# Kernel tuning notes

Measured on AMD Instinct MI355X. Metric: run time of the kernel, lower is better.

## Reference

```python
import jax, jax.numpy as jnp
import numpy as np

SHAPE = (4096, 4096)
TAU = 1.0
EPS = 1e-8


def setup_inputs() -> dict:
    key = jax.random.key(0)
    k1, k2, k3 = jax.random.split(key, 3)
    mask_logits = 0.1 * jax.random.normal(k1, SHAPE, dtype=jnp.float32)
    u1 = jax.random.uniform(k2, SHAPE, dtype=jnp.float32)
    u2 = jax.random.uniform(k3, SHAPE + (2,), dtype=jnp.float32)
    return {"mask_logits": mask_logits, "u1": u1, "u2": u2,
            "k": 1677721, "training": 1}


def _gumbel(u):
    # -log(-log(U + eps) + eps), matching the torch code's noise
    return -jnp.log(-jnp.log(u + EPS) + EPS)


def reference(mask_logits, u1, u2, k, training):
    shape = mask_logits.shape
    if training:
        # gumbel-perturbed logits
        logits_with_noise = (mask_logits + _gumbel(u1)) / TAU
        flat = logits_with_noise.reshape(-1)                 # [N]
        _, top_idx = jax.lax.top_k(flat, k)                  # [k]
        # scatter: binary candidate mask (constant values -> non-diff, as in torch)
        mask = jnp.zeros_like(flat).at[top_idx].set(1.0)     # [N]
        # F.gumbel_softmax(stack([0, mask], -1), tau, hard=True)[..., 1]
        logits2 = jnp.stack([jnp.zeros_like(mask), mask], axis=-1)   # [N, 2]
        g2 = _gumbel(u2.reshape(-1, 2))                      # [N, 2]
        y = jax.nn.softmax((logits2 + g2) / TAU, axis=-1)    # soft sample
        hard = jax.nn.one_hot(jnp.argmax(y, axis=-1), 2, dtype=y.dtype)
        out = (hard + y - jax.lax.stop_gradient(y))[..., 1]  # straight-through
        return out.reshape(shape)
    else:
        flat = mask_logits.reshape(-1)
        _, top_idx = jax.lax.top_k(flat, k)
        mask = jnp.zeros_like(flat).at[top_idx].set(1.0)
        return mask.reshape(shape)
```

## Files before the change

kernel.cpp:

```cpp
#include <hip/hip_runtime.h>
#include <hip/hip_bf16.h>
#include <math.h>
#include <cstdint>

#define FEPS 1e-8f
#define NTHR 256
#define CAND_CAP 4096
#define NREP 32

#define GRID_KEYS 2048
#define GRID_H2   2048
#define GRID_FIN  2048
#define GRID_PART 1024

#define ZMIN 8.0f
#define ZSCALE 128.0f
#define ZBINW 0.0078125f


__device__ __forceinline__ uint32_t f2k(float f) {
    uint32_t b = __float_as_uint(f);
    return (b & 0x80000000u) ? ~b : (b | 0x80000000u);
}

__device__ __forceinline__ float gum_fast(float u) {
    float t = u + FEPS;
    float a = logf(t);
    float w = -a + FEPS;
    float d = logf(w);
    return -d;
}

__device__ __forceinline__ float logCR(float x) {
    return (float)log((double)x);
}
__device__ __forceinline__ float gum_cr(float u) {
    float t = u + FEPS;
    float a = logCR(t);
    float w = -a + FEPS;
    float d = logCR(w);
    return -d;
}

__device__ __forceinline__ float decide_cr(float maskv, float ua, float ub) {
    float G0 = gum_cr(ua);
    float G1 = gum_cr(ub);
    float V1 = maskv + G1;
    float diff = V1 - G0;
    return (diff > 0x1p-25f) ? 1.0f : 0.0f;
}

__device__ __forceinline__ float decide_fast(float mv, float ua, float ub) {
    float w0 = -logf(ua + FEPS) + FEPS;
    float w1 = -logf(ub + FEPS) + FEPS;
    float T = (mv != 0.0f) ? 0.36787944f : 1.0f;
    float rhs = T * w1;
    float q = w0 - rhs;
    if (fabsf(q) > 1e-4f * rhs) return (q > 0.0f) ? 1.0f : 0.0f;
    return decide_cr(mv, ua, ub);
}

__device__ __forceinline__ int zbin(float z) {
    float t = (z + ZMIN) * ZSCALE;
    int b = (int)t;
    if (b < 0) b = 0;
    if (b > 4095) b = 4095;
    return b;
}

__global__ void k_zero(uint32_t* __restrict__ hist1r, uint32_t* __restrict__ hist2,
                       uint32_t* __restrict__ scal, uint32_t* __restrict__ candCount) {
    int i = blockIdx.x * blockDim.x + threadIdx.x;
    int stride = gridDim.x * blockDim.x;
    for (int b = i; b < NREP * 4096; b += stride) hist1r[b] = 0u;
    for (int b = i; b < (1 << 20); b += stride) hist2[b] = 0u;
    if (i < 16) scal[i] = 0u;
    if (i == 0) *candCount = 0u;
}

__global__ void __launch_bounds__(NTHR) k_keys(
        const float* __restrict__ lg, const float* __restrict__ u1,
        const int* __restrict__ trainp, uint32_t* __restrict__ keys,
        uint32_t* __restrict__ hist1r, int N) {
    __shared__ uint32_t h[4096];
    for (int b = threadIdx.x; b < 4096; b += NTHR) h[b] = 0u;
    __syncthreads();
    const int tr = *trainp;
    const int n4 = N >> 2;
    const int nth = gridDim.x * NTHR;
    const float4* lg4 = (const float4*)lg;
    const float4* u14 = (const float4*)u1;
    uint4* k4 = (uint4*)keys;

    int p0 = blockIdx.x * NTHR + threadIdx.x;
    while (p0 + nth < n4) {
        const int p1 = p0 + nth;
        float4 m0 = lg4[p0];
        float4 m1 = lg4[p1];
        float4 a0 = u14[p0];
        float4 a1 = u14[p1];
        float z0, z1, z2, z3, z4, z5, z6, z7;
        if (tr) {
            z0 = m0.x + gum_fast(a0.x); z1 = m0.y + gum_fast(a0.y);
            z2 = m0.z + gum_fast(a0.z); z3 = m0.w + gum_fast(a0.w);
            z4 = m1.x + gum_fast(a1.x); z5 = m1.y + gum_fast(a1.y);
            z6 = m1.z + gum_fast(a1.z); z7 = m1.w + gum_fast(a1.w);
        } else {
            z0 = m0.x; z1 = m0.y; z2 = m0.z; z3 = m0.w;
            z4 = m1.x; z5 = m1.y; z6 = m1.z; z7 = m1.w;
        }
        k4[p0] = make_uint4(f2k(z0), f2k(z1), f2k(z2), f2k(z3));
        k4[p1] = make_uint4(f2k(z4), f2k(z5), f2k(z6), f2k(z7));
        atomicAdd(&h[zbin(z0)], 1u); atomicAdd(&h[zbin(z1)], 1u);
        atomicAdd(&h[zbin(z2)], 1u); atomicAdd(&h[zbin(z3)], 1u);
        atomicAdd(&h[zbin(z4)], 1u); atomicAdd(&h[zbin(z5)], 1u);
        atomicAdd(&h[zbin(z6)], 1u); atomicAdd(&h[zbin(z7)], 1u);
        p0 += 2 * nth;
    }
    if (p0 < n4) {
        float4 m0 = lg4[p0];
        float4 a0 = u14[p0];
        float z0, z1, z2, z3;
        if (tr) {
            z0 = m0.x + gum_fast(a0.x); z1 = m0.y + gum_fast(a0.y);
            z2 = m0.z + gum_fast(a0.z); z3 = m0.w + gum_fast(a0.w);
        } else { z0 = m0.x; z1 = m0.y; z2 = m0.z; z3 = m0.w; }
        k4[p0] = make_uint4(f2k(z0), f2k(z1), f2k(z2), f2k(z3));
        atomicAdd(&h[zbin(z0)], 1u); atomicAdd(&h[zbin(z1)], 1u);
        atomicAdd(&h[zbin(z2)], 1u); atomicAdd(&h[zbin(z3)], 1u);
    }
    for (int i = (n4 << 2) + blockIdx.x * NTHR + threadIdx.x; i < N; i += nth) {
        float m = lg[i], u = u1[i];
        float z = tr ? (m + gum_fast(u)) : m;
        keys[i] = f2k(z);
        atomicAdd(&h[zbin(z)], 1u);
    }
    __syncthreads();
    uint32_t* rep = hist1r + (uint32_t)(blockIdx.x & (NREP - 1)) * 4096u;
    for (int b = threadIdx.x; b < 4096; b += NTHR) {
        uint32_t v = h[b];
        if (v) atomicAdd(&rep[b], v);
    }
}

__global__ void __launch_bounds__(1024) k_scan1(
        const uint32_t* __restrict__ hist1r, const int* __restrict__ kptr,
        uint32_t* __restrict__ scal) {
    __shared__ uint32_t vals[4096];
    __shared__ uint32_t cnt[1024];
    const int t = threadIdx.x;
    uint32_t loc = 0;
    for (int j = 0; j < 4; j++) {
        const int bin = 4095 - (t * 4 + j);
        uint32_t v = 0;
        #pragma unroll
        for (int r = 0; r < NREP; r++) v += hist1r[r * 4096 + bin];
        vals[t * 4 + j] = v;
        loc += v;
    }
    cnt[t] = loc;
    __syncthreads();
    for (int off = 1; off < 1024; off <<= 1) {
        uint32_t add = (t >= off) ? cnt[t - off] : 0u;
        __syncthreads();
        cnt[t] += add;
        __syncthreads();
    }
    const uint32_t K = (uint32_t)(*kptr);
    uint32_t excl = (t > 0) ? cnt[t - 1] : 0u;
    uint32_t incl = cnt[t];
    if (excl < K && K <= incl) {
        uint32_t c = excl;
        for (int j = 0; j < 4; j++) {
            uint32_t v = vals[t * 4 + j];
            if (K <= c + v) {
                int b1 = 4095 - (t * 4 + j);
                float edge = (float)b1 * ZBINW - ZMIN;
                uint32_t kb = f2k(edge) - 2048u;
                scal[0] = kb;
                break;
            }
            c += v;
        }
    }
}

__global__ void __launch_bounds__(NTHR) k_hist2(
        const uint32_t* __restrict__ keys, const uint32_t* __restrict__ scal,
        uint32_t* __restrict__ hist2, uint32_t* __restrict__ gtOut, int N) {
    __shared__ uint32_t red[NTHR];
    const uint32_t kb = scal[0];
    const uint32_t hiB = kb + (1u << 20);
    const int n4 = N >> 2;
    const int tid = blockIdx.x * NTHR + threadIdx.x;
    const int stride = gridDim.x * NTHR;
    const uint4* k4 = (const uint4*)keys;
    uint32_t gt = 0;
    for (int i = tid; i < n4; i += stride) {
        uint4 kk = k4[i];
        uint32_t ks[4] = {kk.x, kk.y, kk.z, kk.w};
        #pragma unroll
        for (int j = 0; j < 4; j++) {
            uint32_t kx = ks[j];
            if (kx >= hiB) gt++;
            else if (kx >= kb) atomicAdd(&hist2[kx - kb], 1u);
        }
    }
    for (int i = (n4 << 2) + tid; i < N; i += stride) {
        uint32_t kx = keys[i];
        if (kx >= hiB) gt++;
        else if (kx >= kb) atomicAdd(&hist2[kx - kb], 1u);
    }
    red[threadIdx.x] = gt;
    __syncthreads();
    for (int off = NTHR / 2; off; off >>= 1) {
        if (threadIdx.x < off) red[threadIdx.x] += red[threadIdx.x + off];
        __syncthreads();
    }
    if (threadIdx.x == 0 && red[0]) atomicAdd(gtOut, red[0]);
}

__global__ void __launch_bounds__(NTHR) k_part(
        const uint32_t* __restrict__ hist2, uint32_t* __restrict__ part) {
    __shared__ uint32_t red[NTHR];
    uint32_t sum = 0;
    const int base = blockIdx.x << 10;
    for (int j = threadIdx.x; j < 1024; j += NTHR) sum += hist2[base + j];
    red[threadIdx.x] = sum;
    __syncthreads();
    for (int off = NTHR / 2; off; off >>= 1) {
        if (threadIdx.x < off) red[threadIdx.x] += red[threadIdx.x + off];
        __syncthreads();
    }
    if (threadIdx.x == 0) part[blockIdx.x] = red[0];
}

__global__ void __launch_bounds__(1024) k_scan2(
        const uint32_t* __restrict__ hist2, const uint32_t* __restrict__ part,
        const int* __restrict__ kptr, uint32_t* __restrict__ scal) {
    __shared__ uint32_t cs[1024];
    __shared__ uint32_t bs[1024];
    __shared__ uint32_t red[1024];
    __shared__ int shI[4];
    const int t = threadIdx.x;
    const uint32_t kb = scal[0];
    const uint32_t GT = scal[1];
    const uint32_t kk1 = (uint32_t)(*kptr) - GT;

    cs[t] = part[1023 - t];
    __syncthreads();
    for (int off = 1; off < 1024; off <<= 1) {
        uint32_t add = (t >= off) ? cs[t - off] : 0u;
        __syncthreads();
        cs[t] += add;
        __syncthreads();
    }
    {
        uint32_t excl = t ? cs[t - 1] : 0u;
        if (excl < kk1 && kk1 <= cs[t]) shI[0] = t;
    }
    __syncthreads();
    const int rp = shI[0];
    const int jc = 1023 - rp;
    const uint32_t gt_chunks = rp ? cs[rp - 1] : 0u;
    const uint32_t kk_in = kk1 - gt_chunks;

    bs[t] = hist2[(jc << 10) + (1023 - t)];
    __syncthreads();
    for (int off = 1; off < 1024; off <<= 1) {
        uint32_t add = (t >= off) ? bs[t - off] : 0u;
        __syncthreads();
        bs[t] += add;
        __syncthreads();
    }
    {
        uint32_t excl = t ? bs[t - 1] : 0u;
        if (excl < kk_in && kk_in <= bs[t]) shI[1] = t;
    }
    __syncthreads();
    const int rq = shI[1];
    const int b2 = (jc << 10) + (1023 - rq);

    int W = 64;
    int lo = 0, hi = 0;
    uint32_t caw = 0;
    while (true) {
        lo = b2 - W; if (lo < 0) lo = 0;
        hi = b2 + W; if (hi > 0xFFFFF) hi = 0xFFFFF;
        uint32_t v = 0;
        for (int b = lo + t; b <= hi; b += 1024) v += hist2[b];
        red[t] = v;
        __syncthreads();
        for (int off = 512; off; off >>= 1) {
            if (t < off) red[t] += red[t + off];
            __syncthreads();
        }
        uint32_t nW = red[0];
        __syncthreads();
        if (nW <= 3500u || W == 0) {
            const int ch = hi >> 10;
            const int chend = (ch << 10) + 1023;
            uint32_t v2 = 0;
            for (int b = hi + 1 + t; b <= chend; b += 1024) v2 += hist2[b];
            red[t] = v2;
            __syncthreads();
            for (int off = 512; off; off >>= 1) {
                if (t < off) red[t] += red[t + off];
                __syncthreads();
            }
            uint32_t inpart = red[0];
            __syncthreads();
            const int rpch = 1023 - ch;
            const uint32_t sufExcl = rpch ? cs[rpch - 1] : 0u;
            caw = GT + sufExcl + inpart;
            break;
        }
        W >>= 1;
    }
    if (t == 0) {
        scal[3] = kb + (uint32_t)lo;
        scal[4] = kb + (uint32_t)hi;
        scal[5] = caw;
    }
}

__global__ void __launch_bounds__(NTHR) k_final(
        uint32_t* __restrict__ keys ,
        const float* __restrict__ u2, const int* __restrict__ trainp,
        const uint32_t* __restrict__ scal,
        uint32_t* __restrict__ candIdx, uint32_t* __restrict__ candCount, int N) {
    const uint32_t klo = scal[3], khi = scal[4];
    const int tr = *trainp;
    const int n4 = N >> 2;
    const int tid = blockIdx.x * NTHR + threadIdx.x;
    const int stride = gridDim.x * NTHR;
    const uint4* kr4 = (const uint4*)keys;
    const float4* u24 = (const float4*)u2;
    float* outf = (float*)keys;

    for (int i = tid; i < n4; i += stride) {
        uint4 kk = kr4[i];
        uint32_t ks[4] = {kk.x, kk.y, kk.z, kk.w};
        float uu[8];
        if (tr) {
            float4 ua = u24[2 * i];
            float4 ub = u24[2 * i + 1];
            uu[0] = ua.x; uu[1] = ua.y; uu[2] = ua.z; uu[3] = ua.w;
            uu[4] = ub.x; uu[5] = ub.y; uu[6] = ub.z; uu[7] = ub.w;
        }
        float res[4];
        bool inw[4];
        bool anyw = false;
        #pragma unroll
        for (int j = 0; j < 4; j++) {
            inw[j] = (ks[j] >= klo) && (ks[j] <= khi);
            anyw |= inw[j];
        }
        #pragma unroll
        for (int j = 0; j < 4; j++) {
            float mv = (ks[j] > khi) ? 1.0f : 0.0f;
            res[j] = (tr && !inw[j]) ? decide_fast(mv, uu[2 * j], uu[2 * j + 1]) : mv;
        }
        if (!anyw) {
            ((float4*)outf)[i] = make_float4(res[0], res[1], res[2], res[3]);
        } else {
            #pragma unroll
            for (int j = 0; j < 4; j++) {
                if (inw[j]) {
                    uint32_t p = atomicAdd(candCount, 1u);
                    if (p < CAND_CAP) candIdx[p] = (uint32_t)(4 * i + j);
                } else {
                    outf[4 * i + j] = res[j];
                }
            }
        }
    }
    for (int i = (n4 << 2) + tid; i < N; i += stride) {
        uint32_t kx = keys[i];
        if (kx >= klo && kx <= khi) {
            uint32_t p = atomicAdd(candCount, 1u);
            if (p < CAND_CAP) candIdx[p] = (uint32_t)i;
            continue;
        }
        float mv = (kx > khi) ? 1.0f : 0.0f;
        outf[i] = tr ? decide_fast(mv, u2[2 * i], u2[2 * i + 1]) : mv;
    }
}

__global__ void __launch_bounds__(NTHR) k_refine(
        const float* __restrict__ lg, const float* __restrict__ u1,
        const float* __restrict__ u2, const int* __restrict__ kptr,
        const int* __restrict__ trainp, const uint32_t* __restrict__ scal,
        const uint32_t* __restrict__ candIdx, const uint32_t* __restrict__ candCount,
        float* __restrict__ out) {
    __shared__ float zs[CAND_CAP];
    __shared__ int is[CAND_CAP];
    const int tr = *trainp;
    int n = (int)(*candCount);
    if (n > CAND_CAP) n = CAND_CAP;
    int npow2 = 64;
    while (npow2 < n) npow2 <<= 1;

    for (int e = threadIdx.x; e < npow2; e += NTHR) {
        if (e < n) {
            int i = (int)candIdx[e];
            float m = lg[i];
            zs[e] = tr ? (m + gum_cr(u1[i])) : m;
            is[e] = i;
        } else {
            zs[e] = -INFINITY;
            is[e] = 0x40000000 + e;
        }
    }
    __syncthreads();

    for (int size = 2; size <= npow2; size <<= 1) {
        for (int str = size >> 1; str > 0; str >>= 1) {
            for (int e = threadIdx.x; e < npow2; e += NTHR) {
                int p = e ^ str;
                if (p > e) {
                    float za = zs[e], zb = zs[p];
                    int ia = is[e], ib = is[p];
                    bool aBefore = (za > zb) || (za == zb && ia < ib);
                    bool descBlock = ((e & size) == 0);
                    if (descBlock ? !aBefore : aBefore) {
                        zs[e] = zb; zs[p] = za;
                        is[e] = ib; is[p] = ia;
                    }
                }
            }
            __syncthreads();
        }
    }

    const int K = *kptr;
    const int caw = (int)scal[5];
    const int R = K - caw;
    for (int e = threadIdx.x; e < n; e += NTHR) {
        int i = is[e];
        float mv = (e < R) ? 1.0f : 0.0f;
        out[i] = tr ? decide_cr(mv, u2[2 * i], u2[2 * i + 1]) : mv;
    }
}

extern "C" void kernel_launch(void* const* d_in, const int* in_sizes, int n_in,
                              void* d_out, int out_size, void* d_ws, size_t ws_size,
                              hipStream_t stream) {
    const float* lg = (const float*)d_in[0];
    const float* u1 = (const float*)d_in[1];
    const float* u2 = (const float*)d_in[2];
    const int* kptr = (const int*)d_in[3];
    const int* trainp = (const int*)d_in[4];
    float* out = (float*)d_out;
    const int N = in_sizes[0];

    uint32_t* keys = (uint32_t*)d_out;

    uint32_t* hist1r = (uint32_t*)d_ws;
    uint32_t* hist2 = hist1r + NREP * 4096;
    uint32_t* part = hist2 + (1u << 20);
    uint32_t* scal = part + 1024;
    uint32_t* candCount = scal + 16;
    uint32_t* candIdx = candCount + 1;

    k_zero<<<dim3(1024), dim3(NTHR), 0, stream>>>(hist1r, hist2, scal, candCount);
    k_keys<<<dim3(GRID_KEYS), dim3(NTHR), 0, stream>>>(lg, u1, trainp, keys, hist1r, N);
    k_scan1<<<dim3(1), dim3(1024), 0, stream>>>(hist1r, kptr, scal);
    k_hist2<<<dim3(GRID_H2), dim3(NTHR), 0, stream>>>(keys, scal, hist2, &scal[1], N);
    k_part<<<dim3(GRID_PART), dim3(NTHR), 0, stream>>>(hist2, part);
    k_scan2<<<dim3(1), dim3(1024), 0, stream>>>(hist2, part, kptr, scal);
    k_final<<<dim3(GRID_FIN), dim3(NTHR), 0, stream>>>(keys, u2, trainp, scal,
                                                       candIdx, candCount, N);
    k_refine<<<dim3(1), dim3(NTHR), 0, stream>>>(lg, u1, u2, kptr, trainp, scal,
                                                 candIdx, candCount, out);
}
```

Before: 164.6 us.

## Replace full key pass with sampled histogram, 2-bit class map, and recompute

The first histogram pass now samples 1/16 of the elements to estimate the threshold bin, scaled by K/16. It no longer writes full 32-bit keys. A second pass recomputes the Gumbel values with a fast approximate log and classifies each element as above, below, or near the threshold, storing a 2-bit class map. It refines exactly only inside a band, and the smaller 2^17 histogram drops the partial-sum kernel. The final pass decides clear cases from raw uniform comparisons and recomputes keys only for near-threshold elements, trading memory traffic for recomputation. The risk is sampling error: if the true threshold falls outside the chosen 2^17-key window, the result is wrong.

```diff
diff --git a/kernel.cpp b/kernel.cpp
--- a/kernel.cpp
+++ b/kernel.cpp
@@ -7,11 +7,13 @@
 #define NTHR 256
 #define CAND_CAP 4096
 #define NREP 32
-
-#define GRID_KEYS 2048
-#define GRID_H2   2048
-#define GRID_FIN  2048
-#define GRID_PART 1024
+#define H2BITS 17
+#define H2SIZE (1u << H2BITS)
+#define BAND 3e-3f
+#define UCMP 1e-3f
+
+#define GRID_MAP 2048
+#define GRID_FIN 2048
 
 #define ZMIN 8.0f
 #define ZSCALE 128.0f
@@ -21,43 +23,54 @@
 __device__ __forceinline__ uint32_t f2k(float f) {
     uint32_t b = __float_as_uint(f);
     return (b & 0x80000000u) ? ~b : (b | 0x80000000u);
+}
+__device__ __forceinline__ float k2f(uint32_t k) {
+    uint32_t b = (k & 0x80000000u) ? (k & 0x7FFFFFFFu) : ~k;
+    return __uint_as_float(b);
 }
 
 __device__ __forceinline__ float gum_fast(float u) {
     float t = u + FEPS;
     float a = logf(t);
     float w = -a + FEPS;
-    float d = logf(w);
-    return -d;
-}
-
-__device__ __forceinline__ float logCR(float x) {
-    return (float)log((double)x);
-}
+    return -logf(w);
+}
+__device__ __forceinline__ float gum_scr(float u) {
+    float t = u + FEPS;
+    float a = __logf(t);
+    float w = -a + FEPS;
+    return -__logf(w);
+}
+
+__device__ __forceinline__ float logCR(float x) { return (float)log((double)x); }
 __device__ __forceinline__ float gum_cr(float u) {
     float t = u + FEPS;
     float a = logCR(t);
     float w = -a + FEPS;
-    float d = logCR(w);
-    return -d;
+    return -logCR(w);
 }
 
 __device__ __forceinline__ float decide_cr(float maskv, float ua, float ub) {
     float G0 = gum_cr(ua);
     float G1 = gum_cr(ub);
-    float V1 = maskv + G1;
-    float diff = V1 - G0;
+    float diff = (maskv + G1) - G0;
     return (diff > 0x1p-25f) ? 1.0f : 0.0f;
 }
 
 __device__ __forceinline__ float decide_fast(float mv, float ua, float ub) {
-    float w0 = -logf(ua + FEPS) + FEPS;
-    float w1 = -logf(ub + FEPS) + FEPS;
+    float w0 = -__logf(ua + FEPS) + FEPS;
+    float w1 = -__logf(ub + FEPS) + FEPS;
     float T = (mv != 0.0f) ? 0.36787944f : 1.0f;
     float rhs = T * w1;
     float q = w0 - rhs;
     if (fabsf(q) > 1e-4f * rhs) return (q > 0.0f) ? 1.0f : 0.0f;
     return decide_cr(mv, ua, ub);
+}
+
+__device__ __forceinline__ float decide0(float ua, float ub) {
+    float d = ub - ua;
+    if (fabsf(d) > UCMP) return (d > 0.0f) ? 1.0f : 0.0f;
+    return decide_fast(0.0f, ua, ub);
 }
 
 __device__ __forceinline__ int zbin(float z) {
@@ -73,67 +86,35 @@
     int i = blockIdx.x * blockDim.x + threadIdx.x;
     int stride = gridDim.x * blockDim.x;
     for (int b = i; b < NREP * 4096; b += stride) hist1r[b] = 0u;
-    for (int b = i; b < (1 << 20); b += stride) hist2[b] = 0u;
+    for (uint32_t b = i; b < H2SIZE; b += stride) hist2[b] = 0u;
     if (i < 16) scal[i] = 0u;
     if (i == 0) *candCount = 0u;
 }
 
-__global__ void __launch_bounds__(NTHR) k_keys(
+__global__ void __launch_bounds__(NTHR) k_samp(
         const float* __restrict__ lg, const float* __restrict__ u1,
-        const int* __restrict__ trainp, uint32_t* __restrict__ keys,
-        uint32_t* __restrict__ hist1r, int N) {
+        const int* __restrict__ trainp, uint32_t* __restrict__ hist1r, int N) {
     __shared__ uint32_t h[4096];
     for (int b = threadIdx.x; b < 4096; b += NTHR) h[b] = 0u;
     __syncthreads();
     const int tr = *trainp;
     const int n4 = N >> 2;
-    const int nth = gridDim.x * NTHR;
+    const int gtid = blockIdx.x * NTHR + threadIdx.x;
     const float4* lg4 = (const float4*)lg;
     const float4* u14 = (const float4*)u1;
-    uint4* k4 = (uint4*)keys;
-
-    int p0 = blockIdx.x * NTHR + threadIdx.x;
-    while (p0 + nth < n4) {
-        const int p1 = p0 + nth;
-        float4 m0 = lg4[p0];
-        float4 m1 = lg4[p1];
-        float4 a0 = u14[p0];
-        float4 a1 = u14[p1];
-        float z0, z1, z2, z3, z4, z5, z6, z7;
-        if (tr) {
-            z0 = m0.x + gum_fast(a0.x); z1 = m0.y + gum_fast(a0.y);
-            z2 = m0.z + gum_fast(a0.z); z3 = m0.w + gum_fast(a0.w);
-            z4 = m1.x + gum_fast(a1.x); z5 = m1.y + gum_fast(a1.y);
-            z6 = m1.z + gum_fast(a1.z); z7 = m1.w + gum_fast(a1.w);
-        } else {
-            z0 = m0.x; z1 = m0.y; z2 = m0.z; z3 = m0.w;
-            z4 = m1.x; z5 = m1.y; z6 = m1.z; z7 = m1.w;
-        }
-        k4[p0] = make_uint4(f2k(z0), f2k(z1), f2k(z2), f2k(z3));
-        k4[p1] = make_uint4(f2k(z4), f2k(z5), f2k(z6), f2k(z7));
-        atomicAdd(&h[zbin(z0)], 1u); atomicAdd(&h[zbin(z1)], 1u);
-        atomicAdd(&h[zbin(z2)], 1u); atomicAdd(&h[zbin(z3)], 1u);
-        atomicAdd(&h[zbin(z4)], 1u); atomicAdd(&h[zbin(z5)], 1u);
-        atomicAdd(&h[zbin(z6)], 1u); atomicAdd(&h[zbin(z7)], 1u);
-        p0 += 2 * nth;
-    }
-    if (p0 < n4) {
-        float4 m0 = lg4[p0];
-        float4 a0 = u14[p0];
-        float z0, z1, z2, z3;
-        if (tr) {
-            z0 = m0.x + gum_fast(a0.x); z1 = m0.y + gum_fast(a0.y);
-            z2 = m0.z + gum_fast(a0.z); z3 = m0.w + gum_fast(a0.w);
-        } else { z0 = m0.x; z1 = m0.y; z2 = m0.z; z3 = m0.w; }
-        k4[p0] = make_uint4(f2k(z0), f2k(z1), f2k(z2), f2k(z3));
-        atomicAdd(&h[zbin(z0)], 1u); atomicAdd(&h[zbin(z1)], 1u);
-        atomicAdd(&h[zbin(z2)], 1u); atomicAdd(&h[zbin(z3)], 1u);
-    }
-    for (int i = (n4 << 2) + blockIdx.x * NTHR + threadIdx.x; i < N; i += nth) {
-        float m = lg[i], u = u1[i];
-        float z = tr ? (m + gum_fast(u)) : m;
-        keys[i] = f2k(z);
-        atomicAdd(&h[zbin(z)], 1u);
+    #pragma unroll
+    for (int q = 0; q < 4; q++) {
+        int pos = (gtid + q * 65536) << 4;
+        if (pos < n4) {
+            float4 m = lg4[pos];
+            float4 u = u14[pos];
+            float z0 = tr ? m.x + gum_scr(u.x) : m.x;
+            float z1 = tr ? m.y + gum_scr(u.y) : m.y;
+            float z2 = tr ? m.z + gum_scr(u.z) : m.z;
+            float z3 = tr ? m.w + gum_scr(u.w) : m.w;
+            atomicAdd(&h[zbin(z0)], 1u); atomicAdd(&h[zbin(z1)], 1u);
+            atomicAdd(&h[zbin(z2)], 1u); atomicAdd(&h[zbin(z3)], 1u);
+        }
     }
     __syncthreads();
     uint32_t* rep = hist1r + (uint32_t)(blockIdx.x & (NREP - 1)) * 4096u;
@@ -166,18 +147,24 @@
         cnt[t] += add;
         __syncthreads();
     }
-    const uint32_t K = (uint32_t)(*kptr);
-    uint32_t excl = (t > 0) ? cnt[t - 1] : 0u;
-    uint32_t incl = cnt[t];
-    if (excl < K && K <= incl) {
-        uint32_t c = excl;
+    const float Kf = (float)(*kptr) * 0.0625f;
+    float excl = (t > 0) ? (float)cnt[t - 1] : 0.0f;
+    float incl = (float)cnt[t];
+    if (excl < Kf && Kf <= incl) {
+        float c = excl;
         for (int j = 0; j < 4; j++) {
-            uint32_t v = vals[t * 4 + j];
-            if (K <= c + v) {
+            float v = (float)vals[t * 4 + j];
+            if (Kf <= c + v) {
                 int b1 = 4095 - (t * 4 + j);
-                float edge = (float)b1 * ZBINW - ZMIN;
-                uint32_t kb = f2k(edge) - 2048u;
+                int bmar = b1 - 2;
+                if (bmar < 0) bmar = 0;
+                float elo = (float)bmar * ZBINW - ZMIN;
+                uint32_t kb = f2k(elo);
                 scal[0] = kb;
+                float zlo = k2f(kb) - BAND;
+                float zhi = k2f(kb + H2SIZE) + BAND;
+                scal[6] = __float_as_uint(zlo);
+                scal[7] = __float_as_uint(zhi);
                 break;
             }
             c += v;
@@ -185,31 +172,75 @@
     }
 }
 
-__global__ void __launch_bounds__(NTHR) k_hist2(
-        const uint32_t* __restrict__ keys, const uint32_t* __restrict__ scal,
-        uint32_t* __restrict__ hist2, uint32_t* __restrict__ gtOut, int N) {
+__global__ void __launch_bounds__(NTHR) k_map(
+        const float* __restrict__ lg, const float* __restrict__ u1,
+        const int* __restrict__ trainp, const uint32_t* __restrict__ scal_ro,
+        uint32_t* __restrict__ hist2, uint32_t* __restrict__ scal,
+        unsigned char* __restrict__ map, int N) {
     __shared__ uint32_t red[NTHR];
-    const uint32_t kb = scal[0];
-    const uint32_t hiB = kb + (1u << 20);
+    const int tr = *trainp;
+    const uint32_t kb = scal_ro[0];
+    const uint32_t hiB = kb + H2SIZE;
+    const float zlo_scr = __uint_as_float(scal_ro[6]);
+    const float zhi_scr = __uint_as_float(scal_ro[7]);
     const int n4 = N >> 2;
-    const int tid = blockIdx.x * NTHR + threadIdx.x;
-    const int stride = gridDim.x * NTHR;
-    const uint4* k4 = (const uint4*)keys;
+    const int nth = gridDim.x * NTHR;
+    const float4* lg4 = (const float4*)lg;
+    const float4* u14 = (const float4*)u1;
     uint32_t gt = 0;
-    for (int i = tid; i < n4; i += stride) {
-        uint4 kk = k4[i];
-        uint32_t ks[4] = {kk.x, kk.y, kk.z, kk.w};
+
+    int p0 = blockIdx.x * NTHR + threadIdx.x;
+    while (p0 + nth < n4) {
+        const int p1 = p0 + nth;
+        float4 m0 = lg4[p0];
+        float4 m1 = lg4[p1];
+        float4 a0 = u14[p0];
+        float4 a1 = u14[p1];
+        float ms[8] = {m0.x, m0.y, m0.z, m0.w, m1.x, m1.y, m1.z, m1.w};
+        float us[8] = {a0.x, a0.y, a0.z, a0.w, a1.x, a1.y, a1.z, a1.w};
+        unsigned int bc0 = 0, bc1 = 0;
+        #pragma unroll
+        for (int j = 0; j < 8; j++) {
+            float zh = tr ? ms[j] + gum_scr(us[j]) : ms[j];
+            uint32_t cls;
+            if (zh > zhi_scr) { cls = 1u; gt++; }
+            else if (zh < zlo_scr) cls = 0u;
+            else {
+                float ze = tr ? ms[j] + gum_fast(us[j]) : ms[j];
+                uint32_t key = f2k(ze);
+                if (key >= hiB) { cls = 1u; gt++; }
+                else if (key >= kb) { atomicAdd(&hist2[key - kb], 1u); cls = 2u; }
+                else cls = 0u;
+            }
+            if (j < 4) bc0 |= cls << (2 * j);
+            else bc1 |= cls << (2 * (j - 4));
+        }
+        map[p0] = (unsigned char)bc0;
+        map[p1] = (unsigned char)bc1;
+        p0 += 2 * nth;
+    }
+    if (p0 < n4) {
+        float4 m0 = lg4[p0];
+        float4 a0 = u14[p0];
+        float ms[4] = {m0.x, m0.y, m0.z, m0.w};
+        float us[4] = {a0.x, a0.y, a0.z, a0.w};
+        unsigned int bc0 = 0;
         #pragma unroll
         for (int j = 0; j < 4; j++) {
-            uint32_t kx = ks[j];
-            if (kx >= hiB) gt++;
-            else if (kx >= kb) atomicAdd(&hist2[kx - kb], 1u);
-        }
-    }
-    for (int i = (n4 << 2) + tid; i < N; i += stride) {
-        uint32_t kx = keys[i];
-        if (kx >= hiB) gt++;
-        else if (kx >= kb) atomicAdd(&hist2[kx - kb], 1u);
+            float zh = tr ? ms[j] + gum_scr(us[j]) : ms[j];
+            uint32_t cls;
+            if (zh > zhi_scr) { cls = 1u; gt++; }
+            else if (zh < zlo_scr) cls = 0u;
+            else {
+                float ze = tr ? ms[j] + gum_fast(us[j]) : ms[j];
+                uint32_t key = f2k(ze);
+                if (key >= hiB) { cls = 1u; gt++; }
+                else if (key >= kb) { atomicAdd(&hist2[key - kb], 1u); cls = 2u; }
+                else cls = 0u;
+            }
+            bc0 |= cls << (2 * j);
+        }
+        map[p0] = (unsigned char)bc0;
     }
     red[threadIdx.x] = gt;
     __syncthreads();
@@ -217,55 +248,44 @@
         if (threadIdx.x < off) red[threadIdx.x] += red[threadIdx.x + off];
         __syncthreads();
     }
-    if (threadIdx.x == 0 && red[0]) atomicAdd(gtOut, red[0]);
-}
-
-__global__ void __launch_bounds__(NTHR) k_part(
-        const uint32_t* __restrict__ hist2, uint32_t* __restrict__ part) {
-    __shared__ uint32_t red[NTHR];
-    uint32_t sum = 0;
-    const int base = blockIdx.x << 10;
-    for (int j = threadIdx.x; j < 1024; j += NTHR) sum += hist2[base + j];
-    red[threadIdx.x] = sum;
-    __syncthreads();
-    for (int off = NTHR / 2; off; off >>= 1) {
-        if (threadIdx.x < off) red[threadIdx.x] += red[threadIdx.x + off];
-        __syncthreads();
-    }
-    if (threadIdx.x == 0) part[blockIdx.x] = red[0];
+    if (threadIdx.x == 0 && red[0]) atomicAdd(&scal[1], red[0]);
 }
 
 __global__ void __launch_bounds__(1024) k_scan2(
-        const uint32_t* __restrict__ hist2, const uint32_t* __restrict__ part,
-        const int* __restrict__ kptr, uint32_t* __restrict__ scal) {
-    __shared__ uint32_t cs[1024];
+        const uint32_t* __restrict__ hist2, const int* __restrict__ kptr,
+        uint32_t* __restrict__ scal) {
+    __shared__ uint32_t ss[1024];
     __shared__ uint32_t bs[1024];
     __shared__ uint32_t red[1024];
-    __shared__ int shI[4];
+    __shared__ int shI[2];
     const int t = threadIdx.x;
     const uint32_t kb = scal[0];
+    if (t < 2) shI[t] = 0;
+
+    const int s = 1023 - t;
+    uint32_t sum = 0;
+    for (int j = 0; j < 128; j++) sum += hist2[(s << 7) + j];
+    ss[t] = sum;
+    __syncthreads();
+    for (int off = 1; off < 1024; off <<= 1) {
+        uint32_t add = (t >= off) ? ss[t - off] : 0u;
+        __syncthreads();
+        ss[t] += add;
+        __syncthreads();
+    }
     const uint32_t GT = scal[1];
     const uint32_t kk1 = (uint32_t)(*kptr) - GT;
-
-    cs[t] = part[1023 - t];
-    __syncthreads();
-    for (int off = 1; off < 1024; off <<= 1) {
-        uint32_t add = (t >= off) ? cs[t - off] : 0u;
-        __syncthreads();
-        cs[t] += add;
-        __syncthreads();
-    }
     {
-        uint32_t excl = t ? cs[t - 1] : 0u;
-        if (excl < kk1 && kk1 <= cs[t]) shI[0] = t;
+        uint32_t excl = t ? ss[t - 1] : 0u;
+        if (excl < kk1 && kk1 <= ss[t]) shI[0] = t;
     }
     __syncthreads();
     const int rp = shI[0];
-    const int jc = 1023 - rp;
-    const uint32_t gt_chunks = rp ? cs[rp - 1] : 0u;
-    const uint32_t kk_in = kk1 - gt_chunks;
-
-    bs[t] = hist2[(jc << 10) + (1023 - t)];
+    const int sstrip = 1023 - rp;
+    const uint32_t gt_strips = rp ? ss[rp - 1] : 0u;
+    const uint32_t kk_in = kk1 - gt_strips;
+
+    bs[t] = (t < 128) ? hist2[(sstrip << 7) + (127 - t)] : 0u;
     __syncthreads();
     for (int off = 1; off < 1024; off <<= 1) {
         uint32_t add = (t >= off) ? bs[t - off] : 0u;
@@ -275,18 +295,18 @@
     }
     {
         uint32_t excl = t ? bs[t - 1] : 0u;
-        if (excl < kk_in && kk_in <= bs[t]) shI[1] = t;
+        if (t < 128 && excl < kk_in && kk_in <= bs[t]) shI[1] = t;
     }
     __syncthreads();
     const int rq = shI[1];
-    const int b2 = (jc << 10) + (1023 - rq);
+    const int b2 = (sstrip << 7) + (127 - rq);
 
     int W = 64;
     int lo = 0, hi = 0;
     uint32_t caw = 0;
     while (true) {
         lo = b2 - W; if (lo < 0) lo = 0;
-        hi = b2 + W; if (hi > 0xFFFFF) hi = 0xFFFFF;
+        hi = b2 + W; if (hi > (int)H2SIZE - 1) hi = (int)H2SIZE - 1;
         uint32_t v = 0;
         for (int b = lo + t; b <= hi; b += 1024) v += hist2[b];
         red[t] = v;
@@ -298,10 +318,10 @@
         uint32_t nW = red[0];
         __syncthreads();
         if (nW <= 3500u || W == 0) {
-            const int ch = hi >> 10;
-            const int chend = (ch << 10) + 1023;
+            const int hs = hi >> 7;
+            const int hend = ((hs + 1) << 7) - 1;
             uint32_t v2 = 0;
-            for (int b = hi + 1 + t; b <= chend; b += 1024) v2 += hist2[b];
+            for (int b = hi + 1 + t; b <= hend; b += 1024) v2 += hist2[b];
             red[t] = v2;
             __syncthreads();
             for (int off = 512; off; off >>= 1) {
@@ -310,9 +330,9 @@
             }
             uint32_t inpart = red[0];
             __syncthreads();
-            const int rpch = 1023 - ch;
-            const uint32_t sufExcl = rpch ? cs[rpch - 1] : 0u;
-            caw = GT + sufExcl + inpart;
+            const int rp_hs = 1023 - hs;
+            const uint32_t strips_above = rp_hs ? ss[rp_hs - 1] : 0u;
+            caw = GT + strips_above + inpart;
             break;
         }
         W >>= 1;
@@ -325,65 +345,68 @@
 }
 
 __global__ void __launch_bounds__(NTHR) k_final(
-        uint32_t* __restrict__ keys ,
+        const unsigned char* __restrict__ map,
+        const float* __restrict__ lg, const float* __restrict__ u1,
         const float* __restrict__ u2, const int* __restrict__ trainp,
         const uint32_t* __restrict__ scal,
-        uint32_t* __restrict__ candIdx, uint32_t* __restrict__ candCount, int N) {
+        uint32_t* __restrict__ candIdx, uint32_t* __restrict__ candCount,
+        float* __restrict__ out, int N) {
     const uint32_t klo = scal[3], khi = scal[4];
     const int tr = *trainp;
     const int n4 = N >> 2;
     const int tid = blockIdx.x * NTHR + threadIdx.x;
     const int stride = gridDim.x * NTHR;
-    const uint4* kr4 = (const uint4*)keys;
     const float4* u24 = (const float4*)u2;
-    float* outf = (float*)keys;
+    const float4* lg4 = (const float4*)lg;
+    const float4* u14 = (const float4*)u1;
 
     for (int i = tid; i < n4; i += stride) {
-        uint4 kk = kr4[i];
-        uint32_t ks[4] = {kk.x, kk.y, kk.z, kk.w};
-        float uu[8];
-        if (tr) {
-            float4 ua = u24[2 * i];
-            float4 ub = u24[2 * i + 1];
-            uu[0] = ua.x; uu[1] = ua.y; uu[2] = ua.z; uu[3] = ua.w;
-            uu[4] = ub.x; uu[5] = ub.y; uu[6] = ub.z; uu[7] = ub.w;
+        const unsigned int b = map[i];
+        float4 ua4, ub4;
+        if (tr) { ua4 = u24[2 * i]; ub4 = u24[2 * i + 1]; }
+        float pa[4] = {ua4.x, ua4.z, ub4.x, ub4.z};
+        float pb[4] = {ua4.y, ua4.w, ub4.y, ub4.w};
+        const bool has2 = ((b & 3u) == 2u) | (((b >> 2) & 3u) == 2u) |
+                          (((b >> 4) & 3u) == 2u) | (((b >> 6) & 3u) == 2u);
+        float me[4], ue[4];
+        if (has2) {
+            float4 mm = lg4[i];
+            float4 uu = u14[i];
+            me[0] = mm.x; me[1] = mm.y; me[2] = mm.z; me[3] = mm.w;
+            ue[0] = uu.x; ue[1] = uu.y; ue[2] = uu.z; ue[3] = uu.w;
         }
         float res[4];
-        bool inw[4];
-        bool anyw = false;
+        bool cand[4];
+        bool anyc = false;
         #pragma unroll
         for (int j = 0; j < 4; j++) {
-            inw[j] = (ks[j] >= klo) && (ks[j] <= khi);
-            anyw |= inw[j];
-        }
-        #pragma unroll
-        for (int j = 0; j < 4; j++) {
-            float mv = (ks[j] > khi) ? 1.0f : 0.0f;
-            res[j] = (tr && !inw[j]) ? decide_fast(mv, uu[2 * j], uu[2 * j + 1]) : mv;
-        }
-        if (!anyw) {
-            ((float4*)outf)[i] = make_float4(res[0], res[1], res[2], res[3]);
+            const unsigned int cls = (b >> (2 * j)) & 3u;
+            cand[j] = false;
+            if (cls == 0u) {
+                res[j] = tr ? decide0(pa[j], pb[j]) : 0.0f;
+            } else if (cls == 1u) {
+                res[j] = tr ? decide_fast(1.0f, pa[j], pb[j]) : 1.0f;
+            } else {
+                float ze = tr ? me[j] + gum_fast(ue[j]) : me[j];
+                uint32_t key = f2k(ze);
+                if (key > khi) res[j] = tr ? decide_fast(1.0f, pa[j], pb[j]) : 1.0f;
+                else if (key < klo) res[j] = tr ? decide0(pa[j], pb[j]) : 0.0f;
+                else { cand[j] = true; anyc = true; res[j] = 0.0f; }
+            }
+        }
+        if (!anyc) {
+            ((float4*)out)[i] = make_float4(res[0], res[1], res[2], res[3]);
         } else {
             #pragma unroll
             for (int j = 0; j < 4; j++) {
-                if (inw[j]) {
+                if (cand[j]) {
                     uint32_t p = atomicAdd(candCount, 1u);
                     if (p < CAND_CAP) candIdx[p] = (uint32_t)(4 * i + j);
                 } else {
-                    outf[4 * i + j] = res[j];
+                    out[4 * i + j] = res[j];
                 }
             }
         }
-    }
-    for (int i = (n4 << 2) + tid; i < N; i += stride) {
-        uint32_t kx = keys[i];
-        if (kx >= klo && kx <= khi) {
-            uint32_t p = atomicAdd(candCount, 1u);
-            if (p < CAND_CAP) candIdx[p] = (uint32_t)i;
-            continue;
-        }
-        float mv = (kx > khi) ? 1.0f : 0.0f;
-        outf[i] = tr ? decide_fast(mv, u2[2 * i], u2[2 * i + 1]) : mv;
     }
 }
 
@@ -454,23 +477,21 @@
     float* out = (float*)d_out;
     const int N = in_sizes[0];
 
-    uint32_t* keys = (uint32_t*)d_out;
-
     uint32_t* hist1r = (uint32_t*)d_ws;
     uint32_t* hist2 = hist1r + NREP * 4096;
-    uint32_t* part = hist2 + (1u << 20);
-    uint32_t* scal = part + 1024;
+    uint32_t* scal = hist2 + H2SIZE;
     uint32_t* candCount = scal + 16;
     uint32_t* candIdx = candCount + 1;
-
-    k_zero<<<dim3(1024), dim3(NTHR), 0, stream>>>(hist1r, hist2, scal, candCount);
-    k_keys<<<dim3(GRID_KEYS), dim3(NTHR), 0, stream>>>(lg, u1, trainp, keys, hist1r, N);
+    unsigned char* map = (unsigned char*)(candIdx + CAND_CAP);
+
+    k_zero<<<dim3(256), dim3(NTHR), 0, stream>>>(hist1r, hist2, scal, candCount);
+    k_samp<<<dim3(256), dim3(NTHR), 0, stream>>>(lg, u1, trainp, hist1r, N);
     k_scan1<<<dim3(1), dim3(1024), 0, stream>>>(hist1r, kptr, scal);
-    k_hist2<<<dim3(GRID_H2), dim3(NTHR), 0, stream>>>(keys, scal, hist2, &scal[1], N);
-    k_part<<<dim3(GRID_PART), dim3(NTHR), 0, stream>>>(hist2, part);
-    k_scan2<<<dim3(1), dim3(1024), 0, stream>>>(hist2, part, kptr, scal);
-    k_final<<<dim3(GRID_FIN), dim3(NTHR), 0, stream>>>(keys, u2, trainp, scal,
-                                                       candIdx, candCount, N);
+    k_map<<<dim3(GRID_MAP), dim3(NTHR), 0, stream>>>(lg, u1, trainp, scal, hist2,
+                                                     scal, map, N);
+    k_scan2<<<dim3(1), dim3(1024), 0, stream>>>(hist2, kptr, scal);
+    k_final<<<dim3(GRID_FIN), dim3(NTHR), 0, stream>>>(map, lg, u1, u2, trainp, scal,
+                                                       candIdx, candCount, out, N);
     k_refine<<<dim3(1), dim3(NTHR), 0, stream>>>(lg, u1, u2, kptr, trainp, scal,
                                                  candIdx, candCount, out);
 }
```

New measurement: 201.4 us. 1.22x slower.
